# Optimization experiments

Hardware: AMD Instinct MI355X
Metric: run time of the kernel (lower is better)

The kernel has to match this reference:

```python
import jax, jax.numpy as jnp
import numpy as np

D_MODEL = 1024
N_EXPERTS = 8
HIDDEN = ((int(round(D_MODEL * (8.0 / 3.0))) + 63) // 64) * 64  # 2752
ALPHA = 0.05  # load_balance_alpha


def setup_inputs() -> dict:
    key = jax.random.key(0)
    ks = jax.random.split(key, 6)
    s = 0.02
    x = jax.random.normal(ks[0], (4, 1024, D_MODEL), dtype=jnp.float32)
    Wg = jax.random.normal(ks[1], (D_MODEL, N_EXPERTS), dtype=jnp.float32) * s
    bg = jnp.zeros((N_EXPERTS,), dtype=jnp.float32)
    Wu = jax.random.normal(ks[2], (N_EXPERTS, D_MODEL, HIDDEN), dtype=jnp.float32) * s
    Wv = jax.random.normal(ks[3], (N_EXPERTS, D_MODEL, HIDDEN), dtype=jnp.float32) * s
    Wd = jax.random.normal(ks[4], (N_EXPERTS, HIDDEN, D_MODEL), dtype=jnp.float32) * s
    return {"x": x, "Wg": Wg, "bg": bg, "Wu": Wu, "Wv": Wv, "Wd": Wd}


def reference(x, Wg, bg, Wu, Wv, Wd):
    b, t, d = x.shape
    E = Wu.shape[0]
    xf = x.reshape(b * t, d)  # [N, d]

    # Top-1 router
    logits = xf @ Wg + bg                      # [N, E]
    probs = jax.nn.softmax(logits, axis=-1)
    top1_idx = jnp.argmax(probs, axis=-1)      # [N]
    top1_p = jnp.max(probs, axis=-1)           # [N]
    onehot = jax.nn.one_hot(top1_idx, E, dtype=x.dtype)  # [N, E]

    # Load-balancing aux loss (both me and ce are under no_grad in the original)
    me = jax.lax.stop_gradient(onehot.mean(axis=0))
    ce = jax.lax.stop_gradient(probs.mean(axis=0))
    aux = ALPHA * E * jnp.sum(me * ce)

    # Dropless dispatch: masked per-expert SwiGLU (loop over small fixed E)
    gate = onehot * top1_p[:, None]            # [N, E] combine weights
    y = jnp.zeros_like(xf)
    for e in range(E):
        u = xf @ Wu[e]                         # [N, H]
        v = xf @ Wv[e]                         # [N, H]
        ye = (jax.nn.silu(u) * v) @ Wd[e]      # [N, d]
        y = y + gate[:, e, None] * ye

    return y.reshape(b, t, d), aux
```

## Files before the change

### kernel.cpp

```cpp
#include <hip/hip_runtime.h>

#define D_MODEL 1024
#define HID     2752
#define NEXP    8
#define NTOK    4096
#define ALPHA   0.05f

#define G1_BLOCKS (8 * 32 * 22)

typedef __bf16 bf16_t;
typedef bf16_t bf16x8 __attribute__((ext_vector_type(8)));
typedef float  f32x4  __attribute__((ext_vector_type(4)));

__device__ inline unsigned short f2bf(float f) {
    unsigned int u = __float_as_uint(f);
    u += 0x7fffu + ((u >> 16) & 1u);
    return (unsigned short)(u >> 16);
}

__device__ inline bf16x8 ldsFrag(const unsigned short* p) {
    union { uint4 u; bf16x8 b; } t;
    t.u = *(const uint4*)p;
    return t.b;
}

__device__ inline void gload_lds16(const void* g, void* l) {
    __builtin_amdgcn_global_load_lds((const __attribute__((address_space(1))) void*)g,
                                     (__attribute__((address_space(3))) void*)l, 16, 0, 0);
}

__global__ __launch_bounds__(256) void transposeUV_kernel(const float* __restrict__ Wu,
                                                          const float* __restrict__ Wv,
                                                          unsigned short* __restrict__ WuT,
                                                          unsigned short* __restrict__ WvT) {
    __shared__ float tile[64 * 65];
    const int z = blockIdx.z;
    const int e = z & 7;
    const float* src = ((z < 8) ? Wu : Wv) + (size_t)e * D_MODEL * HID;
    unsigned short* dst = ((z < 8) ? WuT : WvT) + (size_t)e * D_MODEL * HID;
    const int c0 = blockIdx.x * 64, r0 = blockIdx.y * 64;
    const int tid = threadIdx.x;
#pragma unroll
    for (int j = 0; j < 4; ++j) {
        int f = j * 256 + tid;
        int row = f >> 4, c4 = f & 15;
        float4 v = *(const float4*)(src + (size_t)(r0 + row) * HID + c0 + c4 * 4);
        float* t = &tile[row * 65 + c4 * 4];
        t[0] = v.x; t[1] = v.y; t[2] = v.z; t[3] = v.w;
    }
    __syncthreads();
#pragma unroll
    for (int j = 0; j < 2; ++j) {
        int f = j * 256 + tid;
        int orow = f >> 3, kc = f & 7;
        unsigned short pk[8];
#pragma unroll
        for (int q = 0; q < 8; ++q) pk[q] = f2bf(tile[(kc * 8 + q) * 65 + orow]);
        *(uint4*)(dst + (size_t)(c0 + orow) * D_MODEL + r0 + kc * 8) = *(uint4*)pk;
    }
}

__global__ __launch_bounds__(256) void transpose_kernel(const float* __restrict__ in,
                                                        unsigned short* __restrict__ out,
                                                        int R, int C) {
    __shared__ float tile[64 * 65];
    const int e = blockIdx.z;
    const float* src = in + (size_t)e * R * C;
    unsigned short* dst = out + (size_t)e * R * C;
    const int c0 = blockIdx.x * 64, r0 = blockIdx.y * 64;
    const int tid = threadIdx.x;
#pragma unroll
    for (int j = 0; j < 4; ++j) {
        int f = j * 256 + tid;
        int row = f >> 4, c4 = f & 15;
        float4 v = *(const float4*)(src + (size_t)(r0 + row) * C + c0 + c4 * 4);
        float* t = &tile[row * 65 + c4 * 4];
        t[0] = v.x; t[1] = v.y; t[2] = v.z; t[3] = v.w;
    }
    __syncthreads();
#pragma unroll
    for (int j = 0; j < 2; ++j) {
        int f = j * 256 + tid;
        int orow = f >> 3, kc = f & 7;
        unsigned short pk[8];
#pragma unroll
        for (int q = 0; q < 8; ++q) pk[q] = f2bf(tile[(kc * 8 + q) * 65 + orow]);
        *(uint4*)(dst + (size_t)(c0 + orow) * R + r0 + kc * 8) = *(uint4*)pk;
    }
}

__global__ void router_kernel(const float* __restrict__ x, const float* __restrict__ Wg,
                              const float* __restrict__ bg,
                              int* __restrict__ eidx, float* __restrict__ gate_p,
                              int* __restrict__ counts, float* __restrict__ ce_sum,
                              unsigned short* __restrict__ xbf) {
    __shared__ float ceS[8];
    __shared__ int   cntS[8];
    int tid = threadIdx.x;
    if (tid < 8) { ceS[tid] = 0.f; cntS[tid] = 0; }
    __syncthreads();

    int wid = tid >> 6, lane = tid & 63;
    int t = blockIdx.x * 16 + wid;
    const float* xr = x + (size_t)t * D_MODEL;
    unsigned short* xbr = xbf + (size_t)t * D_MODEL;

    float acc[8];
#pragma unroll
    for (int e = 0; e < 8; ++e) acc[e] = 0.f;

#pragma unroll
    for (int c = 0; c < 4; ++c) {
        int i0 = c * 256 + lane * 4;
        float4 xv = *(const float4*)(xr + i0);
        uint2 pk;
        pk.x = (unsigned)f2bf(xv.x) | ((unsigned)f2bf(xv.y) << 16);
        pk.y = (unsigned)f2bf(xv.z) | ((unsigned)f2bf(xv.w) << 16);
        *(uint2*)(xbr + i0) = pk;
#pragma unroll
        for (int j = 0; j < 4; ++j) {
            const float* wr = Wg + (size_t)(i0 + j) * 8;
            float4 lo = *(const float4*)(wr);
            float4 hi = *(const float4*)(wr + 4);
            float xs = (&xv.x)[j];
            acc[0] += xs * lo.x; acc[1] += xs * lo.y;
            acc[2] += xs * lo.z; acc[3] += xs * lo.w;
            acc[4] += xs * hi.x; acc[5] += xs * hi.y;
            acc[6] += xs * hi.z; acc[7] += xs * hi.w;
        }
    }
#pragma unroll
    for (int e = 0; e < 8; ++e) {
#pragma unroll
        for (int off = 32; off > 0; off >>= 1)
            acc[e] += __shfl_xor(acc[e], off, 64);
    }

    if (lane == 0) {
        float lg[8];
#pragma unroll
        for (int e = 0; e < 8; ++e) lg[e] = acc[e] + bg[e];
        float mx = lg[0]; int am = 0;
#pragma unroll
        for (int e = 1; e < 8; ++e) { if (lg[e] > mx) { mx = lg[e]; am = e; } }
        float ex[8], s = 0.f;
#pragma unroll
        for (int e = 0; e < 8; ++e) { ex[e] = __expf(lg[e] - mx); s += ex[e]; }
        float inv = 1.f / s;
#pragma unroll
        for (int e = 0; e < 8; ++e) atomicAdd(&ceS[e], ex[e] * inv);
        atomicAdd(&cntS[am], 1);
        eidx[t] = am;
        gate_p[t] = ex[am] * inv;
    }
    __syncthreads();
    if (tid < 8) atomicAdd(&ce_sum[tid], ceS[tid]);
    if (tid >= 8 && tid < 16) atomicAdd(&counts[tid - 8], cntS[tid - 8]);
}

__global__ void offsets_aux_kernel(const int* __restrict__ counts, const float* __restrict__ ce_sum,
                                   int* __restrict__ offs, float* __restrict__ aux_out) {
    if (threadIdx.x == 0) {
        int off = 0; float aux = 0.f;
        for (int e = 0; e < 8; ++e) {
            offs[e] = off; off += counts[e];
            aux += ((float)counts[e] / (float)NTOK) * (ce_sum[e] / (float)NTOK);
        }
        aux_out[0] = ALPHA * (float)NEXP * aux;
    }
}

__global__ void scatter_kernel(const int* __restrict__ eidx, const int* __restrict__ offs,
                               int* __restrict__ fill, int* __restrict__ toks) {
    int t = blockIdx.x * 256 + threadIdx.x;
    int e = eidx[t];
    int pos = atomicAdd(&fill[e], 1);
    toks[offs[e] + pos] = t;
}

__global__ __launch_bounds__(256, 2) void gemm1_kernel(
    const unsigned short* __restrict__ WuT, const unsigned short* __restrict__ WvT,
    const unsigned short* __restrict__ xbf,
    const int* __restrict__ toks, const int* __restrict__ counts, const int* __restrict__ offs,
    unsigned short* __restrict__ hbuf) {
    const int id = blockIdx.x;
    const int e  = id & 7;
    const int j  = id >> 3;
    const int mt = j & 31;
    const int nt = j >> 5;
    const int Ne = counts[e];
    if (mt * 128 >= Ne) return;
    const int slot0 = offs[e] + mt * 128;
    const int rowsV = min(128, Ne - mt * 128);
    const int ncol0 = nt * 128;
    const int colsV = min(128, HID - ncol0);

    __shared__ unsigned short As[128 * 64];
    __shared__ unsigned short Bus[128 * 64];
    __shared__ unsigned short Bvs[128 * 64];

    const int tid = threadIdx.x;

    const unsigned short* aS[4];
    const unsigned short* buS[4];
    const unsigned short* bvS[4];
    unsigned short* aD[4];
    unsigned short* buD[4];
    unsigned short* bvD[4];
#pragma unroll
    for (int i = 0; i < 4; ++i) {
        int c = i * 256 + tid;
        int r = c >> 3, ch = c & 7;
        int srcOff = ((ch ^ (r & 7)) * 8);
        int ar = min(r, rowsV - 1);
        int tok = toks[slot0 + ar];
        aS[i] = xbf + (size_t)tok * D_MODEL + srcOff;
        int bn = ncol0 + min(r, colsV - 1);
        buS[i] = WuT + ((size_t)e * HID + bn) * D_MODEL + srcOff;
        bvS[i] = WvT + ((size_t)e * HID + bn) * D_MODEL + srcOff;
        aD[i]  = As  + c * 8;
        buD[i] = Bus + c * 8;
        bvD[i] = Bvs + c * 8;
    }

    f32x4 accU[4][4], accV[4][4];
#pragma unroll
    for (int m = 0; m < 4; ++m)
#pragma unroll
        for (int n = 0; n < 4; ++n) {
            accU[m][n] = (f32x4){0.f, 0.f, 0.f, 0.f};
            accV[m][n] = (f32x4){0.f, 0.f, 0.f, 0.f};
        }

    const int lane = tid & 63;
    const int w = tid >> 6;
    const int rbase = (w >> 1) * 64;
    const int cbase = (w & 1) * 64;
    const int lrow = lane & 15;
    const int lchunk = lane >> 4;

    for (int ks = 0; ks < 16; ++ks) {
#pragma unroll
        for (int i = 0; i < 4; ++i) gload_lds16(aS[i],  aD[i]);
#pragma unroll
        for (int i = 0; i < 4; ++i) gload_lds16(buS[i], buD[i]);
#pragma unroll
        for (int i = 0; i < 4; ++i) gload_lds16(bvS[i], bvD[i]);
#pragma unroll
        for (int i = 0; i < 4; ++i) { aS[i] += 64; buS[i] += 64; bvS[i] += 64; }
        __syncthreads();

#pragma unroll
        for (int kk = 0; kk < 2; ++kk) {
            const int g = kk * 4 + lchunk;
            bf16x8 af[4], bu[4], bv[4];
#pragma unroll
            for (int m = 0; m < 4; ++m) {
                int r = rbase + m * 16 + lrow;
                af[m] = ldsFrag(&As[r * 64 + ((g ^ (r & 7)) * 8)]);
            }
#pragma unroll
            for (int n = 0; n < 4; ++n) {
                int rn = cbase + n * 16 + lrow;
                int off = rn * 64 + ((g ^ (rn & 7)) * 8);
                bu[n] = ldsFrag(&Bus[off]);
                bv[n] = ldsFrag(&Bvs[off]);
            }
#pragma unroll
            for (int m = 0; m < 4; ++m)
#pragma unroll
                for (int n = 0; n < 4; ++n) {
                    accU[m][n] = __builtin_amdgcn_mfma_f32_16x16x32_bf16(af[m], bu[n], accU[m][n], 0, 0, 0);
                    accV[m][n] = __builtin_amdgcn_mfma_f32_16x16x32_bf16(af[m], bv[n], accV[m][n], 0, 0, 0);
                }
        }
        __syncthreads();
    }

#pragma unroll
    for (int m = 0; m < 4; ++m) {
#pragma unroll
        for (int i = 0; i < 4; ++i) {
            int r = rbase + m * 16 + (lane >> 4) * 4 + i;
            if (r >= rowsV) continue;
            size_t rowOff = (size_t)(slot0 + r) * HID + ncol0;
#pragma unroll
            for (int n = 0; n < 4; ++n) {
                int c = cbase + n * 16 + (lane & 15);
                if (c < colsV) {
                    float u = accU[m][n][i];
                    float v = accV[m][n][i];
                    float s = u / (1.f + __expf(-u));
                    hbuf[rowOff + c] = f2bf(s * v);
                }
            }
        }
    }
}


#define G2_STAGE(AS, BS)                                                  \
    {                                                                     \
        _Pragma("unroll")                                                 \
        for (int i = 0; i < 4; ++i) { gload_lds16(aS[i], &AS[aOff[i]]); aS[i] += 64; } \
        _Pragma("unroll")                                                 \
        for (int i = 0; i < 2; ++i) { gload_lds16(bS[i], &BS[bOff[i]]); bS[i] += 64; } \
    }

#define G2_COMPUTE(AS, BS)                                                \
    {                                                                     \
        _Pragma("unroll")                                                 \
        for (int kk = 0; kk < 2; ++kk) {                                  \
            const int g = kk * 4 + lchunk;                                \
            bf16x8 af[4], bf[2];                                          \
            _Pragma("unroll")                                             \
            for (int m = 0; m < 4; ++m) {                                 \
                int r = rbase + m * 16 + lrow;                            \
                af[m] = ldsFrag(&AS[r * 64 + ((g ^ (r & 7)) * 8)]);       \
            }                                                             \
            _Pragma("unroll")                                             \
            for (int n = 0; n < 2; ++n) {                                 \
                int rn = cbase + n * 16 + lrow;                           \
                bf[n] = ldsFrag(&BS[rn * 64 + ((g ^ (rn & 7)) * 8)]);     \
            }                                                             \
            __builtin_amdgcn_s_setprio(1);                                \
            _Pragma("unroll")                                             \
            for (int m = 0; m < 4; ++m)                                   \
                _Pragma("unroll")                                         \
                for (int n = 0; n < 2; ++n)                               \
                    acc[m][n] = __builtin_amdgcn_mfma_f32_16x16x32_bf16(af[m], bf[n], acc[m][n], 0, 0, 0); \
            __builtin_amdgcn_s_setprio(0);                                \
        }                                                                 \
    }

__global__ __launch_bounds__(256, 2) void gemm2_kernel(
    const unsigned short* __restrict__ WdT, const unsigned short* __restrict__ hbuf,
    const int* __restrict__ toks, const int* __restrict__ counts, const int* __restrict__ offs,
    const float* __restrict__ gate_p, float* __restrict__ yout) {
    const int id = blockIdx.x;
    const int e  = id & 7;
    const int j  = id >> 3;
    const int mt = j & 31;
    const int nt = j >> 5;
    const int Ne = counts[e];
    if (mt * 128 >= Ne) return;
    const int slot0 = offs[e] + mt * 128;
    const int rowsV = min(128, Ne - mt * 128);
    const int ncol0 = nt * 64;

    __shared__ unsigned short As0[128 * 64];
    __shared__ unsigned short As1[128 * 64];
    __shared__ unsigned short Bs0[64 * 64];
    __shared__ unsigned short Bs1[64 * 64];

    const int tid = threadIdx.x;

    const unsigned short* aS[4];
    int aOff[4];
#pragma unroll
    for (int i = 0; i < 4; ++i) {
        int c = i * 256 + tid;
        int r = c >> 3, ch = c & 7;
        int srcOff = (ch ^ (r & 7)) * 8;
        int ar = min(r, rowsV - 1);
        aS[i] = hbuf + (size_t)(slot0 + ar) * HID + srcOff;
        aOff[i] = c * 8;
    }
    const unsigned short* bS[2];
    int bOff[2];
#pragma unroll
    for (int i = 0; i < 2; ++i) {
        int c = i * 256 + tid;
        int r = c >> 3, ch = c & 7;
        int srcOff = (ch ^ (r & 7)) * 8;
        bS[i] = WdT + ((size_t)e * D_MODEL + ncol0 + r) * HID + srcOff;
        bOff[i] = c * 8;
    }

    f32x4 acc[4][2];
#pragma unroll
    for (int m = 0; m < 4; ++m)
#pragma unroll
        for (int n = 0; n < 2; ++n) acc[m][n] = (f32x4){0.f, 0.f, 0.f, 0.f};

    const int lane = tid & 63;
    const int w = tid >> 6;
    const int rbase = (w >> 1) * 64;
    const int cbase = (w & 1) * 32;
    const int lrow = lane & 15;
    const int lchunk = lane >> 4;

    G2_STAGE(As0, Bs0);
    __syncthreads();

#pragma unroll 1
    for (int k2 = 0; k2 < 21; ++k2) {
        G2_STAGE(As1, Bs1);
        G2_COMPUTE(As0, Bs0);
        __syncthreads();
        G2_STAGE(As0, Bs0);
        G2_COMPUTE(As1, Bs1);
        __syncthreads();
    }
    G2_COMPUTE(As0, Bs0);

#pragma unroll
    for (int m = 0; m < 4; ++m) {
#pragma unroll
        for (int i = 0; i < 4; ++i) {
            int r = rbase + m * 16 + (lane >> 4) * 4 + i;
            if (r >= rowsV) continue;
            int tok = toks[slot0 + r];
            float p = gate_p[tok];
            float* yrow = yout + (size_t)tok * D_MODEL + ncol0;
#pragma unroll
            for (int n = 0; n < 2; ++n) {
                int c = cbase + n * 16 + (lane & 15);
                yrow[c] = p * acc[m][n][i];
            }
        }
    }
}

extern "C" void kernel_launch(void* const* d_in, const int* in_sizes, int n_in,
                              void* d_out, int out_size, void* d_ws, size_t ws_size,
                              hipStream_t stream) {
    const float* x  = (const float*)d_in[0];
    const float* Wg = (const float*)d_in[1];
    const float* bg = (const float*)d_in[2];
    const float* Wu = (const float*)d_in[3];
    const float* Wv = (const float*)d_in[4];
    const float* Wd = (const float*)d_in[5];
    float* yout = (float*)d_out;
    float* aux_out = yout + (size_t)NTOK * D_MODEL;

    char* ws = (char*)d_ws;
    int*   counts = (int*)(ws + 0);
    int*   offs   = (int*)(ws + 32);
    float* ce_sum = (float*)(ws + 64);
    int*   fill   = (int*)(ws + 96);
    int*   eidx   = (int*)(ws + 128);
    float* gate_p = (float*)(ws + 16512);
    int*   toks   = (int*)(ws + 32896);
    unsigned short* xbf  = (unsigned short*)(ws + 65536);
    unsigned short* hbuf = (unsigned short*)(ws + 8454144);
    unsigned short* WuT  = (unsigned short*)(ws + 30998528);
    unsigned short* WvT  = (unsigned short*)(ws + 76087296);
    unsigned short* WdT  = WuT;

    hipMemsetAsync(ws, 0, 128, stream);
    router_kernel<<<256, 1024, 0, stream>>>(x, Wg, bg, eidx, gate_p, counts, ce_sum, xbf);
    offsets_aux_kernel<<<1, 64, 0, stream>>>(counts, ce_sum, offs, aux_out);
    scatter_kernel<<<16, 256, 0, stream>>>(eidx, offs, fill, toks);
    transposeUV_kernel<<<dim3(HID / 64, D_MODEL / 64, 16), 256, 0, stream>>>(Wu, Wv, WuT, WvT);
    gemm1_kernel<<<G1_BLOCKS, 256, 0, stream>>>(WuT, WvT, xbf, toks, counts, offs, hbuf);
    transpose_kernel<<<dim3(D_MODEL / 64, HID / 64, 8), 256, 0, stream>>>(Wd, WdT, HID, D_MODEL);
    gemm2_kernel<<<8 * 32 * 16, 256, 0, stream>>>(WdT, hbuf, toks, counts, offs, gate_p, yout);
}
```

Measured before the change: 269.0 us.

## Narrow gemm1 N-tile to 64 for occupancy and fuse Wd transpose into one kernel

Shrinks the gemm1 output tile from 128x128 to 128x64 (exactly dividing HID), halving accumulators and LDS so launch bounds can request four blocks per SM, and drops the column bounds checks. It also merges the Wd transpose into the Wu/Wv transpose launch when the workspace is large enough for a separate WdT buffer. Together these aim to raise occupancy and remove a serial kernel launch, at the cost of more A-tile reloads per output column and a larger workspace footprint.

New measurement: 356.7 us. 32.6% more time.

```diff
diff --git a/kernel.cpp b/kernel.cpp
--- a/kernel.cpp
+++ b/kernel.cpp
@@ -6,8 +6,6 @@
 #define NTOK    4096
 #define ALPHA   0.05f
 
-#define G1_BLOCKS (8 * 32 * 22)
-
 typedef __bf16 bf16_t;
 typedef bf16_t bf16x8 __attribute__((ext_vector_type(8)));
 typedef float  f32x4  __attribute__((ext_vector_type(4)));
@@ -29,22 +27,36 @@
                                      (__attribute__((address_space(3))) void*)l, 16, 0, 0);
 }
 
-__global__ __launch_bounds__(256) void transposeUV_kernel(const float* __restrict__ Wu,
-                                                          const float* __restrict__ Wv,
-                                                          unsigned short* __restrict__ WuT,
-                                                          unsigned short* __restrict__ WvT) {
+__global__ __launch_bounds__(256) void transposeAll_kernel(const float* __restrict__ Wu,
+                                                           const float* __restrict__ Wv,
+                                                           const float* __restrict__ Wd,
+                                                           unsigned short* __restrict__ WuT,
+                                                           unsigned short* __restrict__ WvT,
+                                                           unsigned short* __restrict__ WdT) {
     __shared__ float tile[64 * 65];
     const int z = blockIdx.z;
-    const int e = z & 7;
-    const float* src = ((z < 8) ? Wu : Wv) + (size_t)e * D_MODEL * HID;
-    unsigned short* dst = ((z < 8) ? WuT : WvT) + (size_t)e * D_MODEL * HID;
-    const int c0 = blockIdx.x * 64, r0 = blockIdx.y * 64;
     const int tid = threadIdx.x;
+    const float* src;
+    unsigned short* dst;
+    int R, C, r0, c0;
+    if (z < 16) {
+        const int e = z & 7;
+        src = ((z < 8) ? Wu : Wv) + (size_t)e * D_MODEL * HID;
+        dst = ((z < 8) ? WuT : WvT) + (size_t)e * D_MODEL * HID;
+        R = D_MODEL; C = HID;
+        r0 = blockIdx.y * 64; c0 = blockIdx.x * 64;
+    } else {
+        const int e = z - 16;
+        src = Wd + (size_t)e * HID * D_MODEL;
+        dst = WdT + (size_t)e * HID * D_MODEL;
+        R = HID; C = D_MODEL;
+        r0 = blockIdx.x * 64; c0 = blockIdx.y * 64;
+    }
 #pragma unroll
     for (int j = 0; j < 4; ++j) {
         int f = j * 256 + tid;
         int row = f >> 4, c4 = f & 15;
-        float4 v = *(const float4*)(src + (size_t)(r0 + row) * HID + c0 + c4 * 4);
+        float4 v = *(const float4*)(src + (size_t)(r0 + row) * C + c0 + c4 * 4);
         float* t = &tile[row * 65 + c4 * 4];
         t[0] = v.x; t[1] = v.y; t[2] = v.z; t[3] = v.w;
     }
@@ -56,7 +68,7 @@
         unsigned short pk[8];
 #pragma unroll
         for (int q = 0; q < 8; ++q) pk[q] = f2bf(tile[(kc * 8 + q) * 65 + orow]);
-        *(uint4*)(dst + (size_t)(c0 + orow) * D_MODEL + r0 + kc * 8) = *(uint4*)pk;
+        *(uint4*)(dst + (size_t)(c0 + orow) * R + r0 + kc * 8) = *(uint4*)pk;
     }
 }
 
@@ -178,56 +190,57 @@
     toks[offs[e] + pos] = t;
 }
 
-__global__ __launch_bounds__(256, 2) void gemm1_kernel(
+__global__ __launch_bounds__(256, 4) void gemm1_kernel(
     const unsigned short* __restrict__ WuT, const unsigned short* __restrict__ WvT,
     const unsigned short* __restrict__ xbf,
     const int* __restrict__ toks, const int* __restrict__ counts, const int* __restrict__ offs,
     unsigned short* __restrict__ hbuf) {
-    const int id = blockIdx.x;
-    const int e  = id & 7;
-    const int j  = id >> 3;
-    const int mt = j & 31;
-    const int nt = j >> 5;
+    const int e  = blockIdx.z;
+    const int mt = blockIdx.y;
+    const int nt = blockIdx.x;
     const int Ne = counts[e];
     if (mt * 128 >= Ne) return;
     const int slot0 = offs[e] + mt * 128;
     const int rowsV = min(128, Ne - mt * 128);
-    const int ncol0 = nt * 128;
-    const int colsV = min(128, HID - ncol0);
+    const int ncol0 = nt * 64;
 
     __shared__ unsigned short As[128 * 64];
-    __shared__ unsigned short Bus[128 * 64];
-    __shared__ unsigned short Bvs[128 * 64];
+    __shared__ unsigned short Bus[64 * 64];
+    __shared__ unsigned short Bvs[64 * 64];
 
     const int tid = threadIdx.x;
 
     const unsigned short* aS[4];
-    const unsigned short* buS[4];
-    const unsigned short* bvS[4];
     unsigned short* aD[4];
-    unsigned short* buD[4];
-    unsigned short* bvD[4];
 #pragma unroll
     for (int i = 0; i < 4; ++i) {
         int c = i * 256 + tid;
         int r = c >> 3, ch = c & 7;
-        int srcOff = ((ch ^ (r & 7)) * 8);
+        int srcOff = (ch ^ (r & 7)) * 8;
         int ar = min(r, rowsV - 1);
         int tok = toks[slot0 + ar];
         aS[i] = xbf + (size_t)tok * D_MODEL + srcOff;
-        int bn = ncol0 + min(r, colsV - 1);
+        aD[i] = As + c * 8;
+    }
+    const unsigned short *buS[2], *bvS[2];
+    unsigned short *buD[2], *bvD[2];
+#pragma unroll
+    for (int i = 0; i < 2; ++i) {
+        int c = i * 256 + tid;
+        int r = c >> 3, ch = c & 7;
+        int srcOff = (ch ^ (r & 7)) * 8;
+        int bn = ncol0 + r;
         buS[i] = WuT + ((size_t)e * HID + bn) * D_MODEL + srcOff;
         bvS[i] = WvT + ((size_t)e * HID + bn) * D_MODEL + srcOff;
-        aD[i]  = As  + c * 8;
         buD[i] = Bus + c * 8;
         bvD[i] = Bvs + c * 8;
     }
 
-    f32x4 accU[4][4], accV[4][4];
+    f32x4 accU[4][2], accV[4][2];
 #pragma unroll
     for (int m = 0; m < 4; ++m)
 #pragma unroll
-        for (int n = 0; n < 4; ++n) {
+        for (int n = 0; n < 2; ++n) {
             accU[m][n] = (f32x4){0.f, 0.f, 0.f, 0.f};
             accV[m][n] = (f32x4){0.f, 0.f, 0.f, 0.f};
         }
@@ -235,32 +248,31 @@
     const int lane = tid & 63;
     const int w = tid >> 6;
     const int rbase = (w >> 1) * 64;
-    const int cbase = (w & 1) * 64;
+    const int cbase = (w & 1) * 32;
     const int lrow = lane & 15;
     const int lchunk = lane >> 4;
 
     for (int ks = 0; ks < 16; ++ks) {
 #pragma unroll
-        for (int i = 0; i < 4; ++i) gload_lds16(aS[i],  aD[i]);
-#pragma unroll
-        for (int i = 0; i < 4; ++i) gload_lds16(buS[i], buD[i]);
-#pragma unroll
-        for (int i = 0; i < 4; ++i) gload_lds16(bvS[i], bvD[i]);
-#pragma unroll
-        for (int i = 0; i < 4; ++i) { aS[i] += 64; buS[i] += 64; bvS[i] += 64; }
+        for (int i = 0; i < 4; ++i) { gload_lds16(aS[i], aD[i]); aS[i] += 64; }
+#pragma unroll
+        for (int i = 0; i < 2; ++i) {
+            gload_lds16(buS[i], buD[i]); buS[i] += 64;
+            gload_lds16(bvS[i], bvD[i]); bvS[i] += 64;
+        }
         __syncthreads();
 
 #pragma unroll
         for (int kk = 0; kk < 2; ++kk) {
             const int g = kk * 4 + lchunk;
-            bf16x8 af[4], bu[4], bv[4];
+            bf16x8 af[4], bu[2], bv[2];
 #pragma unroll
             for (int m = 0; m < 4; ++m) {
                 int r = rbase + m * 16 + lrow;
                 af[m] = ldsFrag(&As[r * 64 + ((g ^ (r & 7)) * 8)]);
             }
 #pragma unroll
-            for (int n = 0; n < 4; ++n) {
+            for (int n = 0; n < 2; ++n) {
                 int rn = cbase + n * 16 + lrow;
                 int off = rn * 64 + ((g ^ (rn & 7)) * 8);
                 bu[n] = ldsFrag(&Bus[off]);
@@ -269,7 +281,7 @@
 #pragma unroll
             for (int m = 0; m < 4; ++m)
 #pragma unroll
-                for (int n = 0; n < 4; ++n) {
+                for (int n = 0; n < 2; ++n) {
                     accU[m][n] = __builtin_amdgcn_mfma_f32_16x16x32_bf16(af[m], bu[n], accU[m][n], 0, 0, 0);
                     accV[m][n] = __builtin_amdgcn_mfma_f32_16x16x32_bf16(af[m], bv[n], accV[m][n], 0, 0, 0);
                 }
@@ -285,14 +297,12 @@
             if (r >= rowsV) continue;
             size_t rowOff = (size_t)(slot0 + r) * HID + ncol0;
 #pragma unroll
-            for (int n = 0; n < 4; ++n) {
+            for (int n = 0; n < 2; ++n) {
                 int c = cbase + n * 16 + (lane & 15);
-                if (c < colsV) {
-                    float u = accU[m][n][i];
-                    float v = accV[m][n][i];
-                    float s = u / (1.f + __expf(-u));
-                    hbuf[rowOff + c] = f2bf(s * v);
-                }
+                float u = accU[m][n][i];
+                float v = accV[m][n][i];
+                float s = u / (1.f + __expf(-u));
+                hbuf[rowOff + c] = f2bf(s * v);
             }
         }
     }
@@ -446,14 +456,19 @@
     unsigned short* hbuf = (unsigned short*)(ws + 8454144);
     unsigned short* WuT  = (unsigned short*)(ws + 30998528);
     unsigned short* WvT  = (unsigned short*)(ws + 76087296);
-    unsigned short* WdT  = WuT;
+    const size_t WDT_OFF = 121176064;
+    const size_t WDT_SZ  = (size_t)NEXP * D_MODEL * HID * 2;
+    const bool sepWdT = ws_size >= WDT_OFF + WDT_SZ;
+    unsigned short* WdT = sepWdT ? (unsigned short*)(ws + WDT_OFF) : WuT;
 
     hipMemsetAsync(ws, 0, 128, stream);
     router_kernel<<<256, 1024, 0, stream>>>(x, Wg, bg, eidx, gate_p, counts, ce_sum, xbf);
     offsets_aux_kernel<<<1, 64, 0, stream>>>(counts, ce_sum, offs, aux_out);
     scatter_kernel<<<16, 256, 0, stream>>>(eidx, offs, fill, toks);
-    transposeUV_kernel<<<dim3(HID / 64, D_MODEL / 64, 16), 256, 0, stream>>>(Wu, Wv, WuT, WvT);
-    gemm1_kernel<<<G1_BLOCKS, 256, 0, stream>>>(WuT, WvT, xbf, toks, counts, offs, hbuf);
-    transpose_kernel<<<dim3(D_MODEL / 64, HID / 64, 8), 256, 0, stream>>>(Wd, WdT, HID, D_MODEL);
+    transposeAll_kernel<<<dim3(HID / 64, D_MODEL / 64, sepWdT ? 24 : 16), 256, 0, stream>>>(
+        Wu, Wv, Wd, WuT, WvT, WdT);
+    gemm1_kernel<<<dim3(43, 32, 8), 256, 0, stream>>>(WuT, WvT, xbf, toks, counts, offs, hbuf);
+    if (!sepWdT)
+        transpose_kernel<<<dim3(D_MODEL / 64, HID / 64, 8), 256, 0, stream>>>(Wd, WdT, HID, D_MODEL);
     gemm2_kernel<<<8 * 32 * 16, 256, 0, stream>>>(WdT, hbuf, toks, counts, offs, gate_p, yout);
 }
```

## Fuse router and all weight transposes into one prep kernel

Applied to the files above, without the earlier changes.

Merges the router, the Wu/Wv transpose and, when workspace allows, the Wd transpose into a single launch whose blocks are split by id. Wd is written to its own workspace buffer so it no longer has to wait for gemm1 to finish with WuT. The gemm1 grid is also remapped from a flat 1D index to a 3D grid ordered (n-tile, m-tile, expert). The intent is fewer launches and better overlap of the small router work with transposes, at the cost of more workspace and a different block-to-expert ordering for gemm1.

Result: faster. 258.3 us (-4.0%).

```diff
diff --git a/kernel.cpp b/kernel.cpp
--- a/kernel.cpp
+++ b/kernel.cpp
@@ -6,7 +6,9 @@
 #define NTOK    4096
 #define ALPHA   0.05f
 
-#define G1_BLOCKS (8 * 32 * 22)
+#define TILES_UV  (43 * 16 * 16)
+#define TILES_WD  (16 * 43 * 8)
+#define RTR_BLKS  1024
 
 typedef __bf16 bf16_t;
 typedef bf16_t bf16x8 __attribute__((ext_vector_type(8)));
@@ -29,35 +31,123 @@
                                      (__attribute__((address_space(3))) void*)l, 16, 0, 0);
 }
 
-__global__ __launch_bounds__(256) void transposeUV_kernel(const float* __restrict__ Wu,
-                                                          const float* __restrict__ Wv,
-                                                          unsigned short* __restrict__ WuT,
-                                                          unsigned short* __restrict__ WvT) {
-    __shared__ float tile[64 * 65];
-    const int z = blockIdx.z;
-    const int e = z & 7;
-    const float* src = ((z < 8) ? Wu : Wv) + (size_t)e * D_MODEL * HID;
-    unsigned short* dst = ((z < 8) ? WuT : WvT) + (size_t)e * D_MODEL * HID;
-    const int c0 = blockIdx.x * 64, r0 = blockIdx.y * 64;
+__global__ __launch_bounds__(256) void prep_kernel(
+    const float* __restrict__ x, const float* __restrict__ Wg, const float* __restrict__ bg,
+    const float* __restrict__ Wu, const float* __restrict__ Wv, const float* __restrict__ Wd,
+    unsigned short* __restrict__ WuT, unsigned short* __restrict__ WvT,
+    unsigned short* __restrict__ WdT,
+    int* __restrict__ eidx, float* __restrict__ gate_p,
+    int* __restrict__ counts, float* __restrict__ ce_sum,
+    unsigned short* __restrict__ xbf, int nTiles) {
+
+    __shared__ float smem[64 * 65];
+    const int id = blockIdx.x;
     const int tid = threadIdx.x;
-#pragma unroll
-    for (int j = 0; j < 4; ++j) {
-        int f = j * 256 + tid;
-        int row = f >> 4, c4 = f & 15;
-        float4 v = *(const float4*)(src + (size_t)(r0 + row) * HID + c0 + c4 * 4);
-        float* t = &tile[row * 65 + c4 * 4];
-        t[0] = v.x; t[1] = v.y; t[2] = v.z; t[3] = v.w;
-    }
+
+    if (id < nTiles) {
+        const int z  = id / 688;
+        const int rm = id - z * 688;
+        const int bx = rm % 43;
+        const int by = rm / 43;
+        const float* src;
+        unsigned short* dst;
+        int R, C, r0, c0;
+        if (z < 16) {
+            const int e = z & 7;
+            src = ((z < 8) ? Wu : Wv) + (size_t)e * D_MODEL * HID;
+            dst = ((z < 8) ? WuT : WvT) + (size_t)e * D_MODEL * HID;
+            R = D_MODEL; C = HID;
+            r0 = by * 64; c0 = bx * 64;
+        } else {
+            const int e = z - 16;
+            src = Wd + (size_t)e * HID * D_MODEL;
+            dst = WdT + (size_t)e * HID * D_MODEL;
+            R = HID; C = D_MODEL;
+            r0 = bx * 64; c0 = by * 64;
+        }
+#pragma unroll
+        for (int j = 0; j < 4; ++j) {
+            int f = j * 256 + tid;
+            int row = f >> 4, c4 = f & 15;
+            float4 v = *(const float4*)(src + (size_t)(r0 + row) * C + c0 + c4 * 4);
+            float* t = &smem[row * 65 + c4 * 4];
+            t[0] = v.x; t[1] = v.y; t[2] = v.z; t[3] = v.w;
+        }
+        __syncthreads();
+#pragma unroll
+        for (int j = 0; j < 2; ++j) {
+            int f = j * 256 + tid;
+            int orow = f >> 3, kc = f & 7;
+            unsigned short pk[8];
+#pragma unroll
+            for (int q = 0; q < 8; ++q) pk[q] = f2bf(smem[(kc * 8 + q) * 65 + orow]);
+            *(uint4*)(dst + (size_t)(c0 + orow) * R + r0 + kc * 8) = *(uint4*)pk;
+        }
+        return;
+    }
+
+    float* ceS = smem;
+    int*   cntS = (int*)(smem + 8);
+    if (tid < 8) { ceS[tid] = 0.f; cntS[tid] = 0; }
     __syncthreads();
-#pragma unroll
-    for (int j = 0; j < 2; ++j) {
-        int f = j * 256 + tid;
-        int orow = f >> 3, kc = f & 7;
-        unsigned short pk[8];
-#pragma unroll
-        for (int q = 0; q < 8; ++q) pk[q] = f2bf(tile[(kc * 8 + q) * 65 + orow]);
-        *(uint4*)(dst + (size_t)(c0 + orow) * D_MODEL + r0 + kc * 8) = *(uint4*)pk;
-    }
+
+    const int rid = id - nTiles;
+    const int wid = tid >> 6, lane = tid & 63;
+    const int t = rid * 4 + wid;
+    const float* xr = x + (size_t)t * D_MODEL;
+    unsigned short* xbr = xbf + (size_t)t * D_MODEL;
+
+    float acc[8];
+#pragma unroll
+    for (int e = 0; e < 8; ++e) acc[e] = 0.f;
+
+#pragma unroll
+    for (int c = 0; c < 4; ++c) {
+        int i0 = c * 256 + lane * 4;
+        float4 xv = *(const float4*)(xr + i0);
+        uint2 pk;
+        pk.x = (unsigned)f2bf(xv.x) | ((unsigned)f2bf(xv.y) << 16);
+        pk.y = (unsigned)f2bf(xv.z) | ((unsigned)f2bf(xv.w) << 16);
+        *(uint2*)(xbr + i0) = pk;
+#pragma unroll
+        for (int j = 0; j < 4; ++j) {
+            const float* wr = Wg + (size_t)(i0 + j) * 8;
+            float4 lo = *(const float4*)(wr);
+            float4 hi = *(const float4*)(wr + 4);
+            float xs = (&xv.x)[j];
+            acc[0] += xs * lo.x; acc[1] += xs * lo.y;
+            acc[2] += xs * lo.z; acc[3] += xs * lo.w;
+            acc[4] += xs * hi.x; acc[5] += xs * hi.y;
+            acc[6] += xs * hi.z; acc[7] += xs * hi.w;
+        }
+    }
+#pragma unroll
+    for (int e = 0; e < 8; ++e) {
+#pragma unroll
+        for (int off = 32; off > 0; off >>= 1)
+            acc[e] += __shfl_xor(acc[e], off, 64);
+    }
+
+    if (lane == 0) {
+        float lg[8];
+#pragma unroll
+        for (int e = 0; e < 8; ++e) lg[e] = acc[e] + bg[e];
+        float mx = lg[0]; int am = 0;
+#pragma unroll
+        for (int e = 1; e < 8; ++e) { if (lg[e] > mx) { mx = lg[e]; am = e; } }
+        float ex[8], s = 0.f;
+#pragma unroll
+        for (int e = 0; e < 8; ++e) { ex[e] = __expf(lg[e] - mx); s += ex[e]; }
+        float inv = 1.f / s;
+#pragma unroll
+        for (int e = 0; e < 8; ++e) atomicAdd(&ceS[e], ex[e] * inv);
+        atomicAdd(&cntS[am], 1);
+        eidx[t] = am;
+        gate_p[t] = ex[am] * inv;
+    }
+    __syncthreads();
+    if (tid < 8) atomicAdd(&ce_sum[tid], ceS[tid]);
+    if (tid >= 8 && tid < 16) atomicAdd(&counts[tid - 8], cntS[tid - 8]);
 }
 
 __global__ __launch_bounds__(256) void transpose_kernel(const float* __restrict__ in,
@@ -89,75 +179,6 @@
     }
 }
 
-__global__ void router_kernel(const float* __restrict__ x, const float* __restrict__ Wg,
-                              const float* __restrict__ bg,
-                              int* __restrict__ eidx, float* __restrict__ gate_p,
-                              int* __restrict__ counts, float* __restrict__ ce_sum,
-                              unsigned short* __restrict__ xbf) {
-    __shared__ float ceS[8];
-    __shared__ int   cntS[8];
-    int tid = threadIdx.x;
-    if (tid < 8) { ceS[tid] = 0.f; cntS[tid] = 0; }
-    __syncthreads();
-
-    int wid = tid >> 6, lane = tid & 63;
-    int t = blockIdx.x * 16 + wid;
-    const float* xr = x + (size_t)t * D_MODEL;
-    unsigned short* xbr = xbf + (size_t)t * D_MODEL;
-
-    float acc[8];
-#pragma unroll
-    for (int e = 0; e < 8; ++e) acc[e] = 0.f;
-
-#pragma unroll
-    for (int c = 0; c < 4; ++c) {
-        int i0 = c * 256 + lane * 4;
-        float4 xv = *(const float4*)(xr + i0);
-        uint2 pk;
-        pk.x = (unsigned)f2bf(xv.x) | ((unsigned)f2bf(xv.y) << 16);
-        pk.y = (unsigned)f2bf(xv.z) | ((unsigned)f2bf(xv.w) << 16);
-        *(uint2*)(xbr + i0) = pk;
-#pragma unroll
-        for (int j = 0; j < 4; ++j) {
-            const float* wr = Wg + (size_t)(i0 + j) * 8;
-            float4 lo = *(const float4*)(wr);
-            float4 hi = *(const float4*)(wr + 4);
-            float xs = (&xv.x)[j];
-            acc[0] += xs * lo.x; acc[1] += xs * lo.y;
-            acc[2] += xs * lo.z; acc[3] += xs * lo.w;
-            acc[4] += xs * hi.x; acc[5] += xs * hi.y;
-            acc[6] += xs * hi.z; acc[7] += xs * hi.w;
-        }
-    }
-#pragma unroll
-    for (int e = 0; e < 8; ++e) {
-#pragma unroll
-        for (int off = 32; off > 0; off >>= 1)
-            acc[e] += __shfl_xor(acc[e], off, 64);
-    }
-
-    if (lane == 0) {
-        float lg[8];
-#pragma unroll
-        for (int e = 0; e < 8; ++e) lg[e] = acc[e] + bg[e];
-        float mx = lg[0]; int am = 0;
-#pragma unroll
-        for (int e = 1; e < 8; ++e) { if (lg[e] > mx) { mx = lg[e]; am = e; } }
-        float ex[8], s = 0.f;
-#pragma unroll
-        for (int e = 0; e < 8; ++e) { ex[e] = __expf(lg[e] - mx); s += ex[e]; }
-        float inv = 1.f / s;
-#pragma unroll
-        for (int e = 0; e < 8; ++e) atomicAdd(&ceS[e], ex[e] * inv);
-        atomicAdd(&cntS[am], 1);
-        eidx[t] = am;
-        gate_p[t] = ex[am] * inv;
-    }
-    __syncthreads();
-    if (tid < 8) atomicAdd(&ce_sum[tid], ceS[tid]);
-    if (tid >= 8 && tid < 16) atomicAdd(&counts[tid - 8], cntS[tid - 8]);
-}
-
 __global__ void offsets_aux_kernel(const int* __restrict__ counts, const float* __restrict__ ce_sum,
                                    int* __restrict__ offs, float* __restrict__ aux_out) {
     if (threadIdx.x == 0) {
@@ -183,13 +204,11 @@
     const unsigned short* __restrict__ xbf,
     const int* __restrict__ toks, const int* __restrict__ counts, const int* __restrict__ offs,
     unsigned short* __restrict__ hbuf) {
-    const int id = blockIdx.x;
-    const int e  = id & 7;
-    const int j  = id >> 3;
-    const int mt = j & 31;
-    const int nt = j >> 5;
+    const int e = blockIdx.z;
     const int Ne = counts[e];
+    const int mt = blockIdx.y;
     if (mt * 128 >= Ne) return;
+    const int nt = blockIdx.x;
     const int slot0 = offs[e] + mt * 128;
     const int rowsV = min(128, Ne - mt * 128);
     const int ncol0 = nt * 128;
@@ -446,14 +465,21 @@
     unsigned short* hbuf = (unsigned short*)(ws + 8454144);
     unsigned short* WuT  = (unsigned short*)(ws + 30998528);
     unsigned short* WvT  = (unsigned short*)(ws + 76087296);
-    unsigned short* WdT  = WuT;
+    const size_t WDT_OFF = 121176064;
+    const size_t WDT_SZ  = (size_t)NEXP * D_MODEL * HID * 2;
+    const bool sepWdT = ws_size >= WDT_OFF + WDT_SZ;
+    unsigned short* WdT = sepWdT ? (unsigned short*)(ws + WDT_OFF) : WuT;
+
+    const int nTiles = sepWdT ? (TILES_UV + TILES_WD) : TILES_UV;
 
     hipMemsetAsync(ws, 0, 128, stream);
-    router_kernel<<<256, 1024, 0, stream>>>(x, Wg, bg, eidx, gate_p, counts, ce_sum, xbf);
+    prep_kernel<<<nTiles + RTR_BLKS, 256, 0, stream>>>(
+        x, Wg, bg, Wu, Wv, Wd, WuT, WvT, WdT,
+        eidx, gate_p, counts, ce_sum, xbf, nTiles);
     offsets_aux_kernel<<<1, 64, 0, stream>>>(counts, ce_sum, offs, aux_out);
     scatter_kernel<<<16, 256, 0, stream>>>(eidx, offs, fill, toks);
-    transposeUV_kernel<<<dim3(HID / 64, D_MODEL / 64, 16), 256, 0, stream>>>(Wu, Wv, WuT, WvT);
-    gemm1_kernel<<<G1_BLOCKS, 256, 0, stream>>>(WuT, WvT, xbf, toks, counts, offs, hbuf);
-    transpose_kernel<<<dim3(D_MODEL / 64, HID / 64, 8), 256, 0, stream>>>(Wd, WdT, HID, D_MODEL);
+    gemm1_kernel<<<dim3(22, 32, 8), 256, 0, stream>>>(WuT, WvT, xbf, toks, counts, offs, hbuf);
+    if (!sepWdT)
+        transpose_kernel<<<dim3(D_MODEL / 64, HID / 64, 8), 256, 0, stream>>>(Wd, WdT, HID, D_MODEL);
     gemm2_kernel<<<8 * 32 * 16, 256, 0, stream>>>(WdT, hbuf, toks, counts, offs, gate_p, yout);
 }
```
